# Optimization experiments

Hardware: AMD Instinct MI355X
Metric: run time of the kernel (lower is better)

Reference implementation:

```python
import jax, jax.numpy as jnp
import numpy as np

KS = 51           # kernel_size
DENSE_INNER = 2
DIM = 128
B, H, W = 16, 64, 64


def _make_peripheral_coords(radius, dense_inner=2):
    coords = list(range(0, min(radius, dense_inner) + 1))
    v = 1
    while v < radius:
        v *= 2
        if v > dense_inner and v < radius:
            coords.append(v)
    if radius not in coords:
        coords.append(radius)
    return sorted(set(coords))


def _quantise(a, coords):
    q = 0
    for c in coords:
        if c <= a:
            q = c
        else:
            break
    return q


def _build_idx(kernel_size, dense_inner):
    radius = kernel_size // 2
    coords = _make_peripheral_coords(radius, dense_inner)
    signed = [-c for c in reversed(coords[1:])] + list(coords)
    P = len(signed)
    c2i = {c: i for i, c in enumerate(signed)}
    idx = []
    for i in range(kernel_size):
        oi = i - radius
        qi = _quantise(abs(oi), coords)
        ii = c2i[-qi if oi < 0 else qi]
        for j in range(kernel_size):
            oj = j - radius
            qj = _quantise(abs(oj), coords)
            jj = c2i[-qj if oj < 0 else qj]
            idx.append(ii * P + jj)
    return np.asarray(idx, dtype=np.int32), P


IDX_MAP, P = _build_idx(KS, DENSE_INNER)  # idx_map buffer, P == 13


def setup_inputs() -> dict:
    key = jax.random.key(0)
    k1, k2, k3 = jax.random.split(key, 3)
    x = jax.random.normal(k1, (B, DIM, H, W), dtype=jnp.float32)
    # trunc_normal(std=0.02) parameters -> scaled normal is a faithful stand-in
    weight_comp = jax.random.normal(k2, (DIM, P * P), dtype=jnp.float32) * 0.02
    kpe = jax.random.normal(k3, (1, 1, KS, KS), dtype=jnp.float32) * 0.02
    return {"x": x, "weight_comp": weight_comp, "kpe": kpe}


def reference(x, weight_comp, kpe):
    dim = weight_comp.shape[0]
    # gather-expand compressed kernel to dense KxK, add positional kernel
    weight = weight_comp[:, IDX_MAP].reshape(dim, 1, KS, KS) + kpe  # [dim,1,K,K]
    pad = KS // 2
    return jax.lax.conv_general_dilated(
        x, weight,
        window_strides=(1, 1),
        padding=[(pad, pad), (pad, pad)],
        dimension_numbers=("NCHW", "OIHW", "NCHW"),
        feature_group_count=dim,
    )
```

## Files before the change

kernel.cpp:

```cpp
#include <hip/hip_runtime.h>

#define KS 51
#define RAD 25
#define DIM 128
#define HW 64

typedef _Float16 f16x8 __attribute__((ext_vector_type(8)));
typedef float f32x4 __attribute__((ext_vector_type(4)));

__device__ __forceinline__ int qidx(int o) {
  int a = o < 0 ? -o : o;
  int r;
  if (a >= 25)      r = 6;
  else if (a >= 16) r = 5;
  else if (a >= 8)  r = 4;
  else if (a >= 4)  r = 3;
  else if (a >= 2)  r = 2;
  else              r = a;
  return o < 0 ? 6 - r : 6 + r;
}

__launch_bounds__(256, 2)
__global__ void dwconv_mfma(const float* __restrict__ x,
                            const float* __restrict__ comp,
                            const float* __restrict__ kpe,
                            float* __restrict__ out) {
  __shared__ unsigned short xs[2 * 64 * 256];
  __shared__ unsigned short wl[64 * 72];

  const int tid = threadIdx.x;
  const int bid = blockIdx.x;
  const int ch  = bid & 127;
  const int bp  = bid >> 7;

  {
    uint4 z; z.x = z.y = z.z = z.w = 0u;
    uint4* p = (uint4*)xs;
    for (int i = tid; i < (2 * 64 * 256) / 8; i += 256) p[i] = z;
  }
  __syncthreads();

  {
    const float* crow = comp + ch * 169;
    for (int t = tid; t < 64 * 72; t += 256) {
      const int ki = t / 72, kj = t - ki * 72;
      float w = 0.f;
      if (ki < KS && kj < KS)
        w = crow[qidx(ki - RAD) * 13 + qidx(kj - RAD)] + kpe[ki * KS + kj];
      wl[t] = __builtin_bit_cast(unsigned short, (_Float16)w);
    }
  }

  {
    const int ii = tid >> 7, rr = (tid >> 1) & 63, hh = tid & 1;
    const float* src = x + ((size_t)((bp * 2 + ii) * DIM + ch)) * (HW * HW) + rr * HW + hh * 32;
    unsigned short* row = &xs[ii * 16384 + rr * 256];
#pragma unroll
    for (int j = 0; j < 32; ++j) {
      const unsigned short u = __builtin_bit_cast(unsigned short, (_Float16)src[j]);
      const int e = RAD + hh * 32 + j;
      row[e] = u;
      row[128 + e - 1] = u;
    }
  }
  __syncthreads();

  const int wv   = tid >> 6;
  const int lane = tid & 63;
  const int g    = lane >> 4;
  const int Lo   = lane & 15;
  const int wimg = wv >> 1;
  const int c0w  = (wv & 1) * 32;

  const int  pi    = Lo & 1;
  const bool m1    = (Lo & 2) != 0;
  const bool m2    = (Lo & 4) != 0;
  const int  laneA = pi * 128 + 8 * (g + (Lo >> 3));
  const int  lo25  = Lo + RAD;

  f32x4 acc[2][4];
#pragma unroll
  for (int mt = 0; mt < 2; ++mt)
#pragma unroll
    for (int nt = 0; nt < 4; ++nt) acc[mt][nt] = (f32x4){0.f, 0.f, 0.f, 0.f};

  const unsigned short* xrow = &xs[wimg * 16384];
  float* outimg = out + ((size_t)((bp * 2 + wimg) * DIM + ch)) * (HW * HW);

#pragma unroll 1
  for (int s = 0; s < 64; ++s, xrow += 256) {
    if (s >= 1 && s <= 38) {
      const int pb = 39 - s;
      const bool zl = (Lo == (pb & 15));
      const int ntb = pb >> 4;
#pragma unroll
      for (int nt = 0; nt < 4; ++nt)
        if (nt == ntb) {
#pragma unroll
          for (int mt = 0; mt < 2; ++mt)
#pragma unroll
            for (int q = 0; q < 4; ++q)
              acc[mt][nt][q] = zl ? 0.f : acc[mt][nt][q];
        }
    }

    const int lo25s = lo25 + s;

#pragma unroll
    for (int kjc = 0; kjc < 2; ++kjc) {
      f16x8 bf[4];
#pragma unroll
      for (int nt = 0; nt < 4; ++nt) {
        const int rho = (lo25s + 16 * nt) & 63;
        bf[nt] = __builtin_bit_cast(f16x8, *(const uint4*)&wl[rho * 72 + g * 8 + kjc * 32]);
      }
#pragma unroll
      for (int mt = 0; mt < 2; ++mt) {
        const int eoff = laneA + c0w + 16 * mt + 32 * kjc;
        const uint4 da = *(const uint4*)&xrow[eoff];
        const uint4 db = *(const uint4*)&xrow[eoff + 8];
        const unsigned d0 = da.x, d1 = da.y, d2 = da.z, d3 = da.w;
        const unsigned d4 = db.x, d5 = db.y, d6 = db.z, d7 = db.w;
        const unsigned e0 = m2 ? d2 : d0, e1 = m2 ? d3 : d1, e2 = m2 ? d4 : d2,
                       e3 = m2 ? d5 : d3, e4 = m2 ? d6 : d4;
        uint4 sv;
        sv.x = m1 ? e1 : e0; sv.y = m1 ? e2 : e1; sv.z = m1 ? e3 : e2; sv.w = m1 ? e4 : e3;
        const f16x8 af = __builtin_bit_cast(f16x8, sv);
#pragma unroll
        for (int nt = 0; nt < 4; ++nt)
          acc[mt][nt] = __builtin_amdgcn_mfma_f32_16x16x32_f16(af, bf[nt], acc[mt][nt], 0, 0, 0);
      }
    }

    if (s >= 25) {
      const int pf = (89 - s) & 63;
      const int r  = s - 25;
      const bool fl = (Lo == (pf & 15));
      const int ntf = pf >> 4;
      float* orow = outimg + r * 64 + c0w + 4 * g;
#pragma unroll
      for (int nt = 0; nt < 4; ++nt)
        if (nt == ntf && fl) {
          *(float4*)&orow[0]  = make_float4(acc[0][nt][0], acc[0][nt][1], acc[0][nt][2], acc[0][nt][3]);
          *(float4*)&orow[16] = make_float4(acc[1][nt][0], acc[1][nt][1], acc[1][nt][2], acc[1][nt][3]);
        }
    }
  }

#pragma unroll
  for (int p = 1; p <= 25; ++p) {
    const int nt = p >> 4;
    const int r  = 64 - p;
    if (Lo == (p & 15)) {
      float* orow = outimg + r * 64 + c0w + 4 * g;
      *(float4*)&orow[0]  = make_float4(acc[0][nt][0], acc[0][nt][1], acc[0][nt][2], acc[0][nt][3]);
      *(float4*)&orow[16] = make_float4(acc[1][nt][0], acc[1][nt][1], acc[1][nt][2], acc[1][nt][3]);
    }
  }
}

extern "C" void kernel_launch(void* const* d_in, const int* in_sizes, int n_in,
                              void* d_out, int out_size, void* d_ws, size_t ws_size,
                              hipStream_t stream) {
  const float* x    = (const float*)d_in[0];
  const float* comp = (const float*)d_in[1];
  const float* kpe  = (const float*)d_in[2];
  float* out        = (float*)d_out;

  dwconv_mfma<<<dim3(1024), dim3(256), 0, stream>>>(x, comp, kpe, out);
}
```

Baseline: 179.6 us.

## Process four images per block, reuse weight fragments, single-copy LDS rows with alignbit

Each block now handles four batch images of one channel instead of two, and each wave computes two images. That lets the weight B-fragments loaded from LDS be reused across two images' MFMAs. The duplicated odd-shifted copy of each input row is replaced by a single compact row, and the half-element shift is built in registers with alignbit. The global input load is vectorised to float4, and one barrier is merged away. The grid halves to 512 blocks and accumulator register pressure doubles, which may cut occupancy or cause spills, and there are fewer blocks to fill the GPU.

```diff
diff --git a/kernel.cpp b/kernel.cpp
--- a/kernel.cpp
+++ b/kernel.cpp
@@ -4,6 +4,7 @@
 #define RAD 25
 #define DIM 128
 #define HW 64
+#define XSTR 136
 
 typedef _Float16 f16x8 __attribute__((ext_vector_type(8)));
 typedef float f32x4 __attribute__((ext_vector_type(4)));
@@ -20,26 +21,32 @@
   return o < 0 ? 6 - r : 6 + r;
 }
 
+__device__ __forceinline__ unsigned alignsel(unsigned hi, unsigned lo, unsigned sh) {
+#if __has_builtin(__builtin_amdgcn_alignbit)
+  return __builtin_amdgcn_alignbit(hi, lo, sh);
+#else
+  return (unsigned)((((unsigned long long)hi << 32) | (unsigned long long)lo) >> sh);
+#endif
+}
+
 __launch_bounds__(256, 2)
 __global__ void dwconv_mfma(const float* __restrict__ x,
                             const float* __restrict__ comp,
                             const float* __restrict__ kpe,
                             float* __restrict__ out) {
-  __shared__ unsigned short xs[2 * 64 * 256];
+  __shared__ unsigned short xs[4 * 64 * XSTR];
   __shared__ unsigned short wl[64 * 72];
 
   const int tid = threadIdx.x;
   const int bid = blockIdx.x;
   const int ch  = bid & 127;
-  const int bp  = bid >> 7;
+  const int grp = bid >> 7;
 
   {
     uint4 z; z.x = z.y = z.z = z.w = 0u;
     uint4* p = (uint4*)xs;
-    for (int i = tid; i < (2 * 64 * 256) / 8; i += 256) p[i] = z;
-  }
-  __syncthreads();
-
+    for (int i = tid; i < (4 * 64 * XSTR * 2) / 16; i += 256) p[i] = z;
+  }
   {
     const float* crow = comp + ch * 169;
     for (int t = tid; t < 64 * 72; t += 256) {
@@ -50,17 +57,26 @@
       wl[t] = __builtin_bit_cast(unsigned short, (_Float16)w);
     }
   }
+  __syncthreads();
 
   {
-    const int ii = tid >> 7, rr = (tid >> 1) & 63, hh = tid & 1;
-    const float* src = x + ((size_t)((bp * 2 + ii) * DIM + ch)) * (HW * HW) + rr * HW + hh * 32;
-    unsigned short* row = &xs[ii * 16384 + rr * 256];
-#pragma unroll
-    for (int j = 0; j < 32; ++j) {
-      const unsigned short u = __builtin_bit_cast(unsigned short, (_Float16)src[j]);
-      const int e = RAD + hh * 32 + j;
-      row[e] = u;
-      row[128 + e - 1] = u;
+    const int fimg = tid >> 6, frow = tid & 63;
+    const float* src = x + ((size_t)((grp * 4 + fimg) * DIM + ch)) * (HW * HW) + frow * HW;
+    float v[64];
+#pragma unroll
+    for (int j = 0; j < 16; ++j) *(float4*)&v[4 * j] = ((const float4*)src)[j];
+    unsigned* dst32 = (unsigned*)&xs[fimg * (64 * XSTR) + frow * XSTR];
+#pragma unroll
+    for (int k = 0; k < 33; ++k) {
+      float lo, hi;
+      if (k == 0)       { lo = 0.f;       hi = v[0]; }
+      else if (k == 32) { lo = v[63];     hi = 0.f;  }
+      else              { lo = v[2 * k - 1]; hi = v[2 * k]; }
+      h2_pack: ;
+      _Float16 plo = (_Float16)lo, phi = (_Float16)hi;
+      unsigned u = (unsigned)__builtin_bit_cast(unsigned short, plo) |
+                   ((unsigned)__builtin_bit_cast(unsigned short, phi) << 16);
+      dst32[12 + k] = u;
     }
   }
   __syncthreads();
@@ -69,26 +85,30 @@
   const int lane = tid & 63;
   const int g    = lane >> 4;
   const int Lo   = lane & 15;
-  const int wimg = wv >> 1;
   const int c0w  = (wv & 1) * 32;
-
-  const int  pi    = Lo & 1;
-  const bool m1    = (Lo & 2) != 0;
-  const bool m2    = (Lo & 4) != 0;
-  const int  laneA = pi * 128 + 8 * (g + (Lo >> 3));
-  const int  lo25  = Lo + RAD;
-
-  f32x4 acc[2][4];
-#pragma unroll
-  for (int mt = 0; mt < 2; ++mt)
-#pragma unroll
-    for (int nt = 0; nt < 4; ++nt) acc[mt][nt] = (f32x4){0.f, 0.f, 0.f, 0.f};
-
-  const unsigned short* xrow = &xs[wimg * 16384];
-  float* outimg = out + ((size_t)((bp * 2 + wimg) * DIM + ch)) * (HW * HW);
+  const int ip   = (wv >> 1) * 2;
+
+  const bool m1 = (Lo & 2) != 0;
+  const bool m2 = (Lo & 4) != 0;
+  const unsigned sh16 = (unsigned)((Lo & 1) << 4);
+  const int baseoff = 8 * (Lo >> 3) + 8 * g + c0w;
+  const int lo25 = Lo + RAD;
+
+  f32x4 acc[2][2][4];
+#pragma unroll
+  for (int i = 0; i < 2; ++i)
+#pragma unroll
+    for (int mt = 0; mt < 2; ++mt)
+#pragma unroll
+      for (int nt = 0; nt < 4; ++nt) acc[i][mt][nt] = (f32x4){0.f, 0.f, 0.f, 0.f};
+
+  const unsigned short* xb0 = &xs[(ip + 0) * (64 * XSTR)];
+  const unsigned short* xb1 = &xs[(ip + 1) * (64 * XSTR)];
+  float* oimg0 = out + ((size_t)((grp * 4 + ip + 0) * DIM + ch)) * (HW * HW);
+  float* oimg1 = out + ((size_t)((grp * 4 + ip + 1) * DIM + ch)) * (HW * HW);
 
 #pragma unroll 1
-  for (int s = 0; s < 64; ++s, xrow += 256) {
+  for (int s = 0; s < 64; ++s) {
     if (s >= 1 && s <= 38) {
       const int pb = 39 - s;
       const bool zl = (Lo == (pb & 15));
@@ -97,38 +117,50 @@
       for (int nt = 0; nt < 4; ++nt)
         if (nt == ntb) {
 #pragma unroll
-          for (int mt = 0; mt < 2; ++mt)
-#pragma unroll
-            for (int q = 0; q < 4; ++q)
-              acc[mt][nt][q] = zl ? 0.f : acc[mt][nt][q];
+          for (int i = 0; i < 2; ++i)
+#pragma unroll
+            for (int mt = 0; mt < 2; ++mt)
+#pragma unroll
+              for (int q = 0; q < 4; ++q)
+                acc[i][mt][nt][q] = zl ? 0.f : acc[i][mt][nt][q];
         }
     }
 
-    const int lo25s = lo25 + s;
-
-#pragma unroll
-    for (int kjc = 0; kjc < 2; ++kjc) {
-      f16x8 bf[4];
-#pragma unroll
-      for (int nt = 0; nt < 4; ++nt) {
-        const int rho = (lo25s + 16 * nt) & 63;
-        bf[nt] = __builtin_bit_cast(f16x8, *(const uint4*)&wl[rho * 72 + g * 8 + kjc * 32]);
-      }
+    uint4 bf[4][2];
+#pragma unroll
+    for (int nt = 0; nt < 4; ++nt) {
+      const int rho = (lo25 + s + 16 * nt) & 63;
+      const int ro  = rho * 72 + g * 8;
+      bf[nt][0] = *(const uint4*)&wl[ro];
+      bf[nt][1] = *(const uint4*)&wl[ro + 32];
+    }
+
+#pragma unroll
+    for (int i = 0; i < 2; ++i) {
+      const unsigned short* xrow = (i == 0 ? xb0 : xb1) + s * XSTR;
 #pragma unroll
       for (int mt = 0; mt < 2; ++mt) {
-        const int eoff = laneA + c0w + 16 * mt + 32 * kjc;
-        const uint4 da = *(const uint4*)&xrow[eoff];
-        const uint4 db = *(const uint4*)&xrow[eoff + 8];
-        const unsigned d0 = da.x, d1 = da.y, d2 = da.z, d3 = da.w;
-        const unsigned d4 = db.x, d5 = db.y, d6 = db.z, d7 = db.w;
-        const unsigned e0 = m2 ? d2 : d0, e1 = m2 ? d3 : d1, e2 = m2 ? d4 : d2,
-                       e3 = m2 ? d5 : d3, e4 = m2 ? d6 : d4;
-        uint4 sv;
-        sv.x = m1 ? e1 : e0; sv.y = m1 ? e2 : e1; sv.z = m1 ? e3 : e2; sv.w = m1 ? e4 : e3;
-        const f16x8 af = __builtin_bit_cast(f16x8, sv);
-#pragma unroll
-        for (int nt = 0; nt < 4; ++nt)
-          acc[mt][nt] = __builtin_amdgcn_mfma_f32_16x16x32_f16(af, bf[nt], acc[mt][nt], 0, 0, 0);
+#pragma unroll
+        for (int kjc = 0; kjc < 2; ++kjc) {
+          const unsigned short* p = xrow + baseoff + 16 * mt + 32 * kjc;
+          const uint4 da = *(const uint4*)p;
+          const uint4 db = *(const uint4*)(p + 8);
+          const unsigned d0 = da.x, d1 = da.y, d2 = da.z, d3 = da.w;
+          const unsigned d4 = db.x, d5 = db.y, d6 = db.z, d7 = db.w;
+          const unsigned e0 = m1 ? d1 : d0, e1 = m1 ? d2 : d1, e2 = m1 ? d3 : d2,
+                         e3 = m1 ? d4 : d3, e4 = m1 ? d5 : d4, e5 = m1 ? d6 : d5,
+                         e6 = m1 ? d7 : d6;
+          const unsigned f0 = m2 ? e2 : e0, f1 = m2 ? e3 : e1, f2 = m2 ? e4 : e2,
+                         f3 = m2 ? e5 : e3, f4 = m2 ? e6 : e4;
+          uint4 sv;
+          sv.x = alignsel(f1, f0, sh16); sv.y = alignsel(f2, f1, sh16);
+          sv.z = alignsel(f3, f2, sh16); sv.w = alignsel(f4, f3, sh16);
+          const f16x8 af = __builtin_bit_cast(f16x8, sv);
+#pragma unroll
+          for (int nt = 0; nt < 4; ++nt)
+            acc[i][mt][nt] = __builtin_amdgcn_mfma_f32_16x16x32_f16(
+                af, __builtin_bit_cast(f16x8, bf[nt][kjc]), acc[i][mt][nt], 0, 0, 0);
+        }
       }
     }
 
@@ -137,12 +169,15 @@
       const int r  = s - 25;
       const bool fl = (Lo == (pf & 15));
       const int ntf = pf >> 4;
-      float* orow = outimg + r * 64 + c0w + 4 * g;
 #pragma unroll
       for (int nt = 0; nt < 4; ++nt)
         if (nt == ntf && fl) {
-          *(float4*)&orow[0]  = make_float4(acc[0][nt][0], acc[0][nt][1], acc[0][nt][2], acc[0][nt][3]);
-          *(float4*)&orow[16] = make_float4(acc[1][nt][0], acc[1][nt][1], acc[1][nt][2], acc[1][nt][3]);
+          float* o0 = oimg0 + r * 64 + c0w + 4 * g;
+          float* o1 = oimg1 + r * 64 + c0w + 4 * g;
+          *(float4*)&o0[0]  = make_float4(acc[0][0][nt][0], acc[0][0][nt][1], acc[0][0][nt][2], acc[0][0][nt][3]);
+          *(float4*)&o0[16] = make_float4(acc[0][1][nt][0], acc[0][1][nt][1], acc[0][1][nt][2], acc[0][1][nt][3]);
+          *(float4*)&o1[0]  = make_float4(acc[1][0][nt][0], acc[1][0][nt][1], acc[1][0][nt][2], acc[1][0][nt][3]);
+          *(float4*)&o1[16] = make_float4(acc[1][1][nt][0], acc[1][1][nt][1], acc[1][1][nt][2], acc[1][1][nt][3]);
         }
     }
   }
@@ -152,9 +187,12 @@
     const int nt = p >> 4;
     const int r  = 64 - p;
     if (Lo == (p & 15)) {
-      float* orow = outimg + r * 64 + c0w + 4 * g;
-      *(float4*)&orow[0]  = make_float4(acc[0][nt][0], acc[0][nt][1], acc[0][nt][2], acc[0][nt][3]);
-      *(float4*)&orow[16] = make_float4(acc[1][nt][0], acc[1][nt][1], acc[1][nt][2], acc[1][nt][3]);
+      float* o0 = oimg0 + r * 64 + c0w + 4 * g;
+      float* o1 = oimg1 + r * 64 + c0w + 4 * g;
+      *(float4*)&o0[0]  = make_float4(acc[0][0][nt][0], acc[0][0][nt][1], acc[0][0][nt][2], acc[0][0][nt][3]);
+      *(float4*)&o0[16] = make_float4(acc[0][1][nt][0], acc[0][1][nt][1], acc[0][1][nt][2], acc[0][1][nt][3]);
+      *(float4*)&o1[0]  = make_float4(acc[1][0][nt][0], acc[1][0][nt][1], acc[1][0][nt][2], acc[1][0][nt][3]);
+      *(float4*)&o1[16] = make_float4(acc[1][1][nt][0], acc[1][1][nt][1], acc[1][1][nt][2], acc[1][1][nt][3]);
     }
   }
 }
@@ -167,5 +205,5 @@
   const float* kpe  = (const float*)d_in[2];
   float* out        = (float*)d_out;
 
-  dwconv_mfma<<<dim3(1024), dim3(256), 0, stream>>>(x, comp, kpe, out);
-}
+  dwconv_mfma<<<dim3(512), dim3(256), 0, stream>>>(x, comp, kpe, out);
+}
```

Result: faster. 162.5 us (-9.5%).
